# Performance work log

Measured on AMD Instinct MI355X. Metric: run time of the kernel, lower is better.

The kernel has to match this reference:

```python
import jax, jax.numpy as jnp
import numpy as np
import math

L_S = 64  # segment length (factor)


def setup_inputs() -> dict:
    key = jax.random.key(0)
    kq, kk, kv = jax.random.split(key, 3)
    B, L, H, D = 4, 8192, 16, 64
    return {
        "queries": jax.random.normal(kq, (B, L, H, D), dtype=jnp.float32),
        "keys": jax.random.normal(kk, (B, L, H, D), dtype=jnp.float32),
        "values": jax.random.normal(kv, (B, L, H, D), dtype=jnp.float32),
        "attn_mask": 0,
    }


def reference(queries, keys, values, attn_mask):
    B, L, H, D = queries.shape
    Ls = L_S
    M = L // Ls  # L % Ls == 0 by construction, so addition_Q path is a no-op
    scale = 1.0 / math.sqrt(Ls * D)

    # segment: [B, M, Ls, H, D]
    sq = queries.reshape(B, M, Ls, H, D)
    sk = keys.reshape(B, M, Ls, H, D)
    sv = values.reshape(B, M, Ls, H, D)

    # rfft over head dim D, ortho norm -> [B, M, Ls, H, D//2+1] complex
    qf = jnp.fft.rfft(sq, axis=-1, norm="ortho")
    kf = jnp.fft.rfft(sk, axis=-1, norm="ortho")
    vf = jnp.fft.rfft(sv, axis=-1, norm="ortho")

    # complex segment correlation: [B, H, M, M]
    scores = jnp.einsum("bmlhd,bnlhd->bhmn", qf, jnp.conj(kf)) / math.sqrt(D)
    A = jax.nn.softmax(scale * jnp.abs(scores), axis=-1)  # real
    Ac = A.astype(qf.dtype)  # complex with zero imaginary part

    # complex weighted sum of value spectra: [B, M, Ls, H, D//2+1]
    Vf = jnp.einsum("bhmn,bnlhd->bmlhd", Ac, vf)
    V = jnp.fft.irfft(Vf, n=D, axis=-1, norm="ortho")  # real [B, M, Ls, H, D]
    return V.reshape(B, L, H, D)
```

## Files before the change

kernel.cpp:

```cpp
#include <hip/hip_runtime.h>
#include <cstdint>
#include <cstddef>


typedef short bf16x8 __attribute__((ext_vector_type(8)));
typedef float f32x4 __attribute__((ext_vector_type(4)));

__device__ __forceinline__ ushort f2bf(float f) {
    union { float f; uint32_t u; } v; v.f = f;
    uint32_t r = (v.u + 0x7FFFu + ((v.u >> 16) & 1u)) >> 16;
    return (ushort)r;
}

__device__ __forceinline__ float bf2f(ushort h) {
    union { uint32_t u; float f; } v; v.u = ((uint32_t)h) << 16;
    return v.f;
}

__global__ void k_gmat(ushort* __restrict__ GreH, ushort* __restrict__ GreL,
                       ushort* __restrict__ GimH, ushort* __restrict__ GimL) {
    const float lam = 1.0f / 32768.0f;
    const float c = 3.14159265358979323846f / 32.0f;
    for (int e = threadIdx.x + blockIdx.x * blockDim.x; e < 4096; e += blockDim.x * gridDim.x) {
        int d = e >> 6, dp = e & 63;
        int delta = d - dp;
        float re = 0.f, im = 0.f;
        for (int k = 0; k <= 32; ++k) {
            int r = ((k * delta) % 64 + 64) % 64;
            float ang = c * (float)r;
            re += cosf(ang);
            im -= sinf(ang);
        }
        re *= lam; im *= lam;
        ushort rh = f2bf(re);
        GreH[e] = rh;
        GreL[e] = f2bf(re - bf2f(rh));
        ushort ih = f2bf(im);
        GimH[e] = ih;
        GimL[e] = f2bf(im - bf2f(ih));
    }
}

__global__ __launch_bounds__(256) void k_prep_q(const float* __restrict__ Q, ushort* __restrict__ Qf) {
    int blk = blockIdx.x;
    int bh = blk >> 7, m = blk & 127;
    int b = bh >> 4, h = bh & 15;
    const float* qbase = Q + ((size_t)(b * 8192 + m * 64)) * 1024 + h * 64;
    ushort* obase = Qf + ((size_t)bh * 128 + m) * 4096;
    for (int idx = threadIdx.x; idx < 1024; idx += 256) {
        int l = idx >> 4, d4 = (idx & 15) * 4;
        float4 v = *(const float4*)(qbase + (size_t)l * 1024 + d4);
        ushort4 o; o.x = f2bf(v.x); o.y = f2bf(v.y); o.z = f2bf(v.z); o.w = f2bf(v.w);
        *(ushort4*)(obase + idx * 4) = o;
    }
}

__global__ __launch_bounds__(256) void k_prep_k(const float* __restrict__ K,
                                                const ushort* __restrict__ GreH,
                                                const ushort* __restrict__ GreL,
                                                const ushort* __restrict__ GimH,
                                                const ushort* __restrict__ GimL,
                                                ushort* __restrict__ Kre, ushort* __restrict__ Kim) {
    __shared__ ushort kb[64 * 72];
    int blk = blockIdx.x;
    int bh = blk >> 7, n = blk & 127;
    int b = bh >> 4, h = bh & 15;
    int t = threadIdx.x;
    int lane = t & 63, wave = t >> 6;
    int wm = wave >> 1, wn = wave & 1;
    int row16 = lane & 15, quad = lane >> 4;

    bf16x8 grh[2][2], grl[2][2], gih[2][2], gil[2][2];
    #pragma unroll
    for (int nt = 0; nt < 2; ++nt)
        #pragma unroll
        for (int kk = 0; kk < 2; ++kk) {
            int off = (wn * 32 + nt * 16 + row16) * 64 + kk * 32 + quad * 8;
            grh[nt][kk] = *(const bf16x8*)(GreH + off);
            grl[nt][kk] = *(const bf16x8*)(GreL + off);
            gih[nt][kk] = *(const bf16x8*)(GimH + off);
            gil[nt][kk] = *(const bf16x8*)(GimL + off);
        }

    {
        int rrow = t >> 2, rcol = (t & 3) * 16;
        const float* kbase = K + ((size_t)(b * 8192 + n * 64 + rrow)) * 1024 + h * 64 + rcol;
        ushort* lbase = &kb[rrow * 72 + rcol];
        #pragma unroll
        for (int c = 0; c < 4; ++c) {
            float4 v = *(const float4*)(kbase + c * 4);
            ushort4 o; o.x = f2bf(v.x); o.y = f2bf(v.y); o.z = f2bf(v.z); o.w = f2bf(v.w);
            *(ushort4*)(lbase + c * 4) = o;
        }
    }
    __syncthreads();

    f32x4 accre[2][2] = {};
    f32x4 accim[2][2] = {};
    #pragma unroll
    for (int kk = 0; kk < 2; ++kk) {
        bf16x8 a[2];
        #pragma unroll
        for (int mt = 0; mt < 2; ++mt)
            a[mt] = *(const bf16x8*)&kb[(wm * 32 + mt * 16 + row16) * 72 + kk * 32 + quad * 8];
        #pragma unroll
        for (int mt = 0; mt < 2; ++mt)
            #pragma unroll
            for (int nt = 0; nt < 2; ++nt) {
                accre[mt][nt] = __builtin_amdgcn_mfma_f32_16x16x32_bf16(a[mt], grh[nt][kk], accre[mt][nt], 0, 0, 0);
                accre[mt][nt] = __builtin_amdgcn_mfma_f32_16x16x32_bf16(a[mt], grl[nt][kk], accre[mt][nt], 0, 0, 0);
                accim[mt][nt] = __builtin_amdgcn_mfma_f32_16x16x32_bf16(a[mt], gih[nt][kk], accim[mt][nt], 0, 0, 0);
                accim[mt][nt] = __builtin_amdgcn_mfma_f32_16x16x32_bf16(a[mt], gil[nt][kk], accim[mt][nt], 0, 0, 0);
            }
    }

    ushort* reb = Kre + ((size_t)bh * 128 + n) * 4096;
    ushort* imb = Kim + ((size_t)bh * 128 + n) * 4096;
    #pragma unroll
    for (int mt = 0; mt < 2; ++mt)
        #pragma unroll
        for (int nt = 0; nt < 2; ++nt)
            #pragma unroll
            for (int i = 0; i < 4; ++i) {
                int l = wm * 32 + mt * 16 + quad * 4 + i;
                int d = wn * 32 + nt * 16 + row16;
                reb[l * 64 + d] = f2bf(accre[mt][nt][i]);
                imb[l * 64 + d] = f2bf(accim[mt][nt][i]);
            }
}

__global__ __launch_bounds__(256) void k_scores(const ushort* __restrict__ Qf,
                                                const ushort* __restrict__ Kre,
                                                const ushort* __restrict__ Kim,
                                                float* __restrict__ Sre, float* __restrict__ Sim) {
    __shared__ ushort qt[64 * 72], ret[64 * 72], imt[64 * 72];
    int bh = blockIdx.y;
    int mh = blockIdx.x >> 1, nh = blockIdx.x & 1;
    int m0 = mh * 64, n0 = nh * 64;
    int t = threadIdx.x;
    int lane = t & 63, wave = t >> 6;
    int wm = wave >> 1, wn = wave & 1;
    int row16 = lane & 15, quad = lane >> 4;
    f32x4 accre[2][2] = {};
    f32x4 accim[2][2] = {};
    const ushort* qg = Qf + ((size_t)bh * 128 + m0) * 4096;
    const ushort* rg = Kre + ((size_t)bh * 128 + n0) * 4096;
    const ushort* ig = Kim + ((size_t)bh * 128 + n0) * 4096;
    for (int kt = 0; kt < 64; ++kt) {
        int j0 = kt * 64;
        #pragma unroll
        for (int p = 0; p < 2; ++p) {
            int idx = p * 256 + t;
            int row = idx >> 3, ch = idx & 7;
            size_t go = (size_t)row * 4096 + j0 + ch * 8;
            int lo = row * 72 + ch * 8;
            *(uint4*)&qt[lo]  = *(const uint4*)(qg + go);
            *(uint4*)&ret[lo] = *(const uint4*)(rg + go);
            *(uint4*)&imt[lo] = *(const uint4*)(ig + go);
        }
        __syncthreads();
        #pragma unroll
        for (int kk = 0; kk < 2; ++kk) {
            bf16x8 a[2], br[2], bi[2];
            #pragma unroll
            for (int mt = 0; mt < 2; ++mt)
                a[mt] = *(const bf16x8*)&qt[(wm * 32 + mt * 16 + row16) * 72 + kk * 32 + quad * 8];
            #pragma unroll
            for (int nt = 0; nt < 2; ++nt) {
                br[nt] = *(const bf16x8*)&ret[(wn * 32 + nt * 16 + row16) * 72 + kk * 32 + quad * 8];
                bi[nt] = *(const bf16x8*)&imt[(wn * 32 + nt * 16 + row16) * 72 + kk * 32 + quad * 8];
            }
            #pragma unroll
            for (int mt = 0; mt < 2; ++mt)
                #pragma unroll
                for (int nt = 0; nt < 2; ++nt) {
                    accre[mt][nt] = __builtin_amdgcn_mfma_f32_16x16x32_bf16(a[mt], br[nt], accre[mt][nt], 0, 0, 0);
                    accim[mt][nt] = __builtin_amdgcn_mfma_f32_16x16x32_bf16(a[mt], bi[nt], accim[mt][nt], 0, 0, 0);
                }
        }
        __syncthreads();
    }
    float* sre = Sre + (size_t)bh * 16384;
    float* sim = Sim + (size_t)bh * 16384;
    #pragma unroll
    for (int mt = 0; mt < 2; ++mt)
        #pragma unroll
        for (int nt = 0; nt < 2; ++nt)
            #pragma unroll
            for (int i = 0; i < 4; ++i) {
                int r = m0 + wm * 32 + mt * 16 + quad * 4 + i;
                int c = n0 + wn * 32 + nt * 16 + row16;
                sre[r * 128 + c] = accre[mt][nt][i];
                sim[r * 128 + c] = accim[mt][nt][i];
            }
}

__global__ __launch_bounds__(128) void k_softmax(const float* __restrict__ Sre,
                                                 const float* __restrict__ Sim,
                                                 ushort* __restrict__ A) {
    __shared__ float redmax[2], redsum[2];
    int row = blockIdx.x;
    int t = threadIdx.x;
    size_t off = (size_t)row * 128 + t;
    float re = Sre[off], im = Sim[off];
    float lg = sqrtf(re * re + im * im);
    float v = lg;
    for (int o = 32; o > 0; o >>= 1) v = fmaxf(v, __shfl_xor(v, o));
    if ((t & 63) == 0) redmax[t >> 6] = v;
    __syncthreads();
    float mx = fmaxf(redmax[0], redmax[1]);
    float e = expf(lg - mx);
    float s = e;
    for (int o = 32; o > 0; o >>= 1) s += __shfl_xor(s, o);
    if ((t & 63) == 0) redsum[t >> 6] = s;
    __syncthreads();
    float tot = redsum[0] + redsum[1];
    A[off] = f2bf(e / tot);
}

__global__ __launch_bounds__(256) void k_vt(const float* __restrict__ V, ushort* __restrict__ Vt) {
    __shared__ float tile[64 * 68];
    int l = blockIdx.x, nh = blockIdx.y, bh = blockIdx.z;
    int b = bh >> 4, h = bh & 15;
    int t = threadIdx.x;
    int n = t & 63, dq = t >> 6;
    const float* vbase = V + ((size_t)(b * 8192 + (nh * 64 + n) * 64 + l)) * 1024 + h * 64;
    #pragma unroll
    for (int r = 0; r < 4; ++r) {
        int d0 = r * 16 + dq * 4;
        float4 v = *(const float4*)(vbase + d0);
        tile[(d0 + 0) * 68 + n] = v.x; tile[(d0 + 1) * 68 + n] = v.y;
        tile[(d0 + 2) * 68 + n] = v.z; tile[(d0 + 3) * 68 + n] = v.w;
    }
    __syncthreads();
    int d = t >> 2, cq = t & 3;
    __align__(16) ushort u[16];
    #pragma unroll
    for (int i = 0; i < 16; ++i) u[i] = f2bf(tile[d * 68 + cq * 16 + i]);
    ushort* ob = Vt + ((size_t)bh * 4096 + l * 64 + d) * 128 + nh * 64 + cq * 16;
    *(uint4*)(ob) = *(uint4*)&u[0];
    *(uint4*)(ob + 8) = *(uint4*)&u[8];
}

__global__ __launch_bounds__(256) void k_mix(const ushort* __restrict__ A,
                                             const ushort* __restrict__ Vt,
                                             float* __restrict__ Out) {
    __shared__ ushort At[128 * 136], Vtl[64 * 136];
    int jt = blockIdx.x, bh = blockIdx.y;
    int b = bh >> 4, h = bh & 15;
    int j0 = jt * 64;
    int t = threadIdx.x;
    int lane = t & 63, wave = t >> 6;
    int row16 = lane & 15, quad = lane >> 4;
    const ushort* ag = A + (size_t)bh * 16384;
    const ushort* vg = Vt + ((size_t)bh * 4096 + j0) * 128;
    #pragma unroll
    for (int p = 0; p < 8; ++p) {
        int idx = p * 256 + t;
        int row = idx >> 4, ch = idx & 15;
        *(uint4*)&At[row * 136 + ch * 8] = *(const uint4*)(ag + row * 128 + ch * 8);
    }
    #pragma unroll
    for (int p = 0; p < 4; ++p) {
        int idx = p * 256 + t;
        int row = idx >> 4, ch = idx & 15;
        *(uint4*)&Vtl[row * 136 + ch * 8] = *(const uint4*)(vg + (size_t)row * 128 + ch * 8);
    }
    __syncthreads();
    f32x4 acc[2][4] = {};
    #pragma unroll
    for (int kk = 0; kk < 4; ++kk) {
        bf16x8 a[2], bv[4];
        #pragma unroll
        for (int mt = 0; mt < 2; ++mt)
            a[mt] = *(const bf16x8*)&At[(wave * 32 + mt * 16 + row16) * 136 + kk * 32 + quad * 8];
        #pragma unroll
        for (int j2 = 0; j2 < 4; ++j2)
            bv[j2] = *(const bf16x8*)&Vtl[(j2 * 16 + row16) * 136 + kk * 32 + quad * 8];
        #pragma unroll
        for (int mt = 0; mt < 2; ++mt)
            #pragma unroll
            for (int j2 = 0; j2 < 4; ++j2)
                acc[mt][j2] = __builtin_amdgcn_mfma_f32_16x16x32_bf16(a[mt], bv[j2], acc[mt][j2], 0, 0, 0);
    }
    #pragma unroll
    for (int mt = 0; mt < 2; ++mt)
        #pragma unroll
        for (int j2 = 0; j2 < 4; ++j2)
            #pragma unroll
            for (int i = 0; i < 4; ++i) {
                int m = wave * 32 + mt * 16 + quad * 4 + i;
                int j = j0 + j2 * 16 + row16;
                int ll = j >> 6, d = j & 63;
                Out[((size_t)(b * 8192 + m * 64 + ll)) * 1024 + h * 64 + d] = acc[mt][j2][i];
            }
}

extern "C" void kernel_launch(void* const* d_in, const int* in_sizes, int n_in,
                              void* d_out, int out_size, void* d_ws, size_t ws_size,
                              hipStream_t stream) {
    const float* Q = (const float*)d_in[0];
    const float* K = (const float*)d_in[1];
    const float* V = (const float*)d_in[2];
    float* Out = (float*)d_out;
    char* ws = (char*)d_ws;
    ushort* GreH = (ushort*)ws;
    ushort* GreL = GreH + 4096;
    ushort* GimH = GreL + 4096;
    ushort* GimL = GimH + 4096;
    float* Sre  = (float*)(ws + 32768);
    float* Sim  = (float*)(ws + 32768 + 4194304);
    ushort* A   = (ushort*)(ws + 32768 + 2 * 4194304);
    ushort* Qf  = (ushort*)(ws + 32768 + 2 * 4194304 + 2097152);
    ushort* Kre = Qf + 33554432;
    ushort* Kim = Kre + 33554432;
    ushort* Vt  = Qf;

    k_gmat<<<16, 256, 0, stream>>>(GreH, GreL, GimH, GimL);
    k_prep_q<<<8192, 256, 0, stream>>>(Q, Qf);
    k_prep_k<<<8192, 256, 0, stream>>>(K, GreH, GreL, GimH, GimL, Kre, Kim);
    k_scores<<<dim3(4, 64), 256, 0, stream>>>(Qf, Kre, Kim, Sre, Sim);
    k_softmax<<<8192, 128, 0, stream>>>(Sre, Sim, A);
    k_vt<<<dim3(64, 2, 64), 256, 0, stream>>>(V, Vt);
    k_mix<<<dim3(64, 64), 256, 0, stream>>>(A, Vt, Out);
}
```

Baseline: 619.4 us.

## Replace real-part DFT matmul with raw K plus DC/Nyquist correction terms

The real part of the frequency-domain score is now computed from raw bf16 K, with two extra appended columns per row (parity-split sums for the DC and Nyquist corrections) instead of a dense real DFT matmul. This removes the Kre matmul and its store. The change also adds register prefetching in k_scores, has each block process several tiles in prep, vt, softmax and mix, and rewrites softmax as one wave per row. The appended columns and rescaling change numerics slightly, and the larger per-block work lowers grid parallelism.

```diff
diff --git a/kernel.cpp b/kernel.cpp
--- a/kernel.cpp
+++ b/kernel.cpp
@@ -17,120 +17,131 @@
     return v.f;
 }
 
-__global__ void k_gmat(ushort* __restrict__ GreH, ushort* __restrict__ GreL,
-                       ushort* __restrict__ GimH, ushort* __restrict__ GimL) {
+__global__ void k_gmat(ushort* __restrict__ GimH, ushort* __restrict__ GimL) {
     const float lam = 1.0f / 32768.0f;
     const float c = 3.14159265358979323846f / 32.0f;
     for (int e = threadIdx.x + blockIdx.x * blockDim.x; e < 4096; e += blockDim.x * gridDim.x) {
         int d = e >> 6, dp = e & 63;
         int delta = d - dp;
-        float re = 0.f, im = 0.f;
+        float im = 0.f;
         for (int k = 0; k <= 32; ++k) {
             int r = ((k * delta) % 64 + 64) % 64;
-            float ang = c * (float)r;
-            re += cosf(ang);
-            im -= sinf(ang);
-        }
-        re *= lam; im *= lam;
-        ushort rh = f2bf(re);
-        GreH[e] = rh;
-        GreL[e] = f2bf(re - bf2f(rh));
+            im -= sinf(c * (float)r);
+        }
+        im *= lam;
         ushort ih = f2bf(im);
         GimH[e] = ih;
         GimL[e] = f2bf(im - bf2f(ih));
     }
 }
 
+#define PSCALE 0.17677669529663687f
+
 __global__ __launch_bounds__(256) void k_prep_q(const float* __restrict__ Q, ushort* __restrict__ Qf) {
-    int blk = blockIdx.x;
-    int bh = blk >> 7, m = blk & 127;
-    int b = bh >> 4, h = bh & 15;
-    const float* qbase = Q + ((size_t)(b * 8192 + m * 64)) * 1024 + h * 64;
-    ushort* obase = Qf + ((size_t)bh * 128 + m) * 4096;
-    for (int idx = threadIdx.x; idx < 1024; idx += 256) {
-        int l = idx >> 4, d4 = (idx & 15) * 4;
-        float4 v = *(const float4*)(qbase + (size_t)l * 1024 + d4);
-        ushort4 o; o.x = f2bf(v.x); o.y = f2bf(v.y); o.z = f2bf(v.z); o.w = f2bf(v.w);
-        *(ushort4*)(obase + idx * 4) = o;
+    int t = threadIdx.x;
+    for (int it = 0; it < 8; ++it) {
+        int g = blockIdx.x * 8 + it;
+        int bh = g >> 7, m = g & 127;
+        int b = bh >> 4, h = bh & 15;
+        const float* qbase = Q + ((size_t)(b * 8192 + m * 64)) * 1024 + h * 64;
+        ushort* obase = Qf + ((size_t)bh * 128 + m) * 4224;
+        #pragma unroll
+        for (int k = 0; k < 4; ++k) {
+            int idx = k * 256 + t;
+            int l = idx >> 4, d4 = (idx & 15) * 4;
+            float4 v = *(const float4*)(qbase + (size_t)l * 1024 + d4);
+            ushort4 o; o.x = f2bf(v.x); o.y = f2bf(v.y); o.z = f2bf(v.z); o.w = f2bf(v.w);
+            *(ushort4*)(obase + l * 64 + d4) = o;
+            float pe = v.x + v.z, po = v.y + v.w;
+            pe += __shfl_xor(pe, 1); po += __shfl_xor(po, 1);
+            pe += __shfl_xor(pe, 2); po += __shfl_xor(po, 2);
+            pe += __shfl_xor(pe, 4); po += __shfl_xor(po, 4);
+            pe += __shfl_xor(pe, 8); po += __shfl_xor(po, 8);
+            if ((t & 15) == 0) {
+                ushort2 pp; pp.x = f2bf(pe * PSCALE); pp.y = f2bf(po * PSCALE);
+                *(ushort2*)(obase + 4096 + 2 * l) = pp;
+            }
+        }
     }
 }
 
 __global__ __launch_bounds__(256) void k_prep_k(const float* __restrict__ K,
-                                                const ushort* __restrict__ GreH,
-                                                const ushort* __restrict__ GreL,
                                                 const ushort* __restrict__ GimH,
                                                 const ushort* __restrict__ GimL,
-                                                ushort* __restrict__ Kre, ushort* __restrict__ Kim) {
+                                                ushort* __restrict__ Kf, ushort* __restrict__ Kim) {
     __shared__ ushort kb[64 * 72];
-    int blk = blockIdx.x;
-    int bh = blk >> 7, n = blk & 127;
-    int b = bh >> 4, h = bh & 15;
     int t = threadIdx.x;
     int lane = t & 63, wave = t >> 6;
     int wm = wave >> 1, wn = wave & 1;
     int row16 = lane & 15, quad = lane >> 4;
-
-    bf16x8 grh[2][2], grl[2][2], gih[2][2], gil[2][2];
+    int rrow = t >> 2, rcol = (t & 3) * 16;
+
+    bf16x8 gih[2][2], gil[2][2];
     #pragma unroll
     for (int nt = 0; nt < 2; ++nt)
         #pragma unroll
         for (int kk = 0; kk < 2; ++kk) {
             int off = (wn * 32 + nt * 16 + row16) * 64 + kk * 32 + quad * 8;
-            grh[nt][kk] = *(const bf16x8*)(GreH + off);
-            grl[nt][kk] = *(const bf16x8*)(GreL + off);
             gih[nt][kk] = *(const bf16x8*)(GimH + off);
             gil[nt][kk] = *(const bf16x8*)(GimL + off);
         }
 
-    {
-        int rrow = t >> 2, rcol = (t & 3) * 16;
+    for (int it = 0; it < 8; ++it) {
+        int g = blockIdx.x * 8 + it;
+        int bh = g >> 7, n = g & 127;
+        int b = bh >> 4, h = bh & 15;
         const float* kbase = K + ((size_t)(b * 8192 + n * 64 + rrow)) * 1024 + h * 64 + rcol;
-        ushort* lbase = &kb[rrow * 72 + rcol];
+        ushort* kfrow = Kf + ((size_t)bh * 128 + n) * 4224;
+        float pe = 0.f, po = 0.f;
         #pragma unroll
         for (int c = 0; c < 4; ++c) {
             float4 v = *(const float4*)(kbase + c * 4);
             ushort4 o; o.x = f2bf(v.x); o.y = f2bf(v.y); o.z = f2bf(v.z); o.w = f2bf(v.w);
-            *(ushort4*)(lbase + c * 4) = o;
-        }
-    }
-    __syncthreads();
-
-    f32x4 accre[2][2] = {};
-    f32x4 accim[2][2] = {};
-    #pragma unroll
-    for (int kk = 0; kk < 2; ++kk) {
-        bf16x8 a[2];
+            *(ushort4*)&kb[rrow * 72 + rcol + c * 4] = o;
+            *(ushort4*)(kfrow + rrow * 64 + rcol + c * 4) = o;
+            pe += v.x + v.z; po += v.y + v.w;
+        }
+        pe += __shfl_xor(pe, 1); po += __shfl_xor(po, 1);
+        pe += __shfl_xor(pe, 2); po += __shfl_xor(po, 2);
+        if ((t & 3) == 0) {
+            ushort2 pp; pp.x = f2bf(pe * PSCALE); pp.y = f2bf(po * PSCALE);
+            *(ushort2*)(kfrow + 4096 + 2 * rrow) = pp;
+        }
+        __syncthreads();
+
+        f32x4 acc[2][2] = {};
+        #pragma unroll
+        for (int kk = 0; kk < 2; ++kk) {
+            bf16x8 a[2];
+            #pragma unroll
+            for (int mt = 0; mt < 2; ++mt)
+                a[mt] = *(const bf16x8*)&kb[(wm * 32 + mt * 16 + row16) * 72 + kk * 32 + quad * 8];
+            #pragma unroll
+            for (int mt = 0; mt < 2; ++mt)
+                #pragma unroll
+                for (int nt = 0; nt < 2; ++nt) {
+                    acc[mt][nt] = __builtin_amdgcn_mfma_f32_16x16x32_bf16(a[mt], gih[nt][kk], acc[mt][nt], 0, 0, 0);
+                    acc[mt][nt] = __builtin_amdgcn_mfma_f32_16x16x32_bf16(a[mt], gil[nt][kk], acc[mt][nt], 0, 0, 0);
+                }
+        }
+        __syncthreads();
         #pragma unroll
         for (int mt = 0; mt < 2; ++mt)
-            a[mt] = *(const bf16x8*)&kb[(wm * 32 + mt * 16 + row16) * 72 + kk * 32 + quad * 8];
-        #pragma unroll
-        for (int mt = 0; mt < 2; ++mt)
-            #pragma unroll
-            for (int nt = 0; nt < 2; ++nt) {
-                accre[mt][nt] = __builtin_amdgcn_mfma_f32_16x16x32_bf16(a[mt], grh[nt][kk], accre[mt][nt], 0, 0, 0);
-                accre[mt][nt] = __builtin_amdgcn_mfma_f32_16x16x32_bf16(a[mt], grl[nt][kk], accre[mt][nt], 0, 0, 0);
-                accim[mt][nt] = __builtin_amdgcn_mfma_f32_16x16x32_bf16(a[mt], gih[nt][kk], accim[mt][nt], 0, 0, 0);
-                accim[mt][nt] = __builtin_amdgcn_mfma_f32_16x16x32_bf16(a[mt], gil[nt][kk], accim[mt][nt], 0, 0, 0);
-            }
-    }
-
-    ushort* reb = Kre + ((size_t)bh * 128 + n) * 4096;
-    ushort* imb = Kim + ((size_t)bh * 128 + n) * 4096;
-    #pragma unroll
-    for (int mt = 0; mt < 2; ++mt)
-        #pragma unroll
-        for (int nt = 0; nt < 2; ++nt)
-            #pragma unroll
-            for (int i = 0; i < 4; ++i) {
-                int l = wm * 32 + mt * 16 + quad * 4 + i;
-                int d = wn * 32 + nt * 16 + row16;
-                reb[l * 64 + d] = f2bf(accre[mt][nt][i]);
-                imb[l * 64 + d] = f2bf(accim[mt][nt][i]);
-            }
+            #pragma unroll
+            for (int nt = 0; nt < 2; ++nt)
+                #pragma unroll
+                for (int i = 0; i < 4; ++i)
+                    kb[(wm * 32 + mt * 16 + quad * 4 + i) * 72 + wn * 32 + nt * 16 + row16] = f2bf(acc[mt][nt][i]);
+        __syncthreads();
+        ushort* kimrow = Kim + ((size_t)bh * 128 + n) * 4096;
+        *(uint4*)(kimrow + rrow * 64 + rcol)     = *(uint4*)&kb[rrow * 72 + rcol];
+        *(uint4*)(kimrow + rrow * 64 + rcol + 8) = *(uint4*)&kb[rrow * 72 + rcol + 8];
+        __syncthreads();
+    }
 }
 
 __global__ __launch_bounds__(256) void k_scores(const ushort* __restrict__ Qf,
-                                                const ushort* __restrict__ Kre,
+                                                const ushort* __restrict__ Kf,
                                                 const ushort* __restrict__ Kim,
                                                 float* __restrict__ Sre, float* __restrict__ Sim) {
     __shared__ ushort qt[64 * 72], ret[64 * 72], imt[64 * 72];
@@ -141,24 +152,43 @@
     int lane = t & 63, wave = t >> 6;
     int wm = wave >> 1, wn = wave & 1;
     int row16 = lane & 15, quad = lane >> 4;
+    const ushort* qg = Qf + ((size_t)bh * 128 + m0) * 4224;
+    const ushort* rg = Kf + ((size_t)bh * 128 + n0) * 4224;
+    const ushort* ig = Kim + ((size_t)bh * 128 + n0) * 4096;
+    uint4 rq[2], rk[2], ri[2];
+    #pragma unroll
+    for (int p = 0; p < 2; ++p) {
+        int idx = p * 256 + t;
+        int row = idx >> 3, ch = idx & 7;
+        rq[p] = *(const uint4*)(qg + (size_t)row * 4224 + ch * 8);
+        rk[p] = *(const uint4*)(rg + (size_t)row * 4224 + ch * 8);
+        ri[p] = *(const uint4*)(ig + (size_t)row * 4096 + ch * 8);
+    }
     f32x4 accre[2][2] = {};
     f32x4 accim[2][2] = {};
-    const ushort* qg = Qf + ((size_t)bh * 128 + m0) * 4096;
-    const ushort* rg = Kre + ((size_t)bh * 128 + n0) * 4096;
-    const ushort* ig = Kim + ((size_t)bh * 128 + n0) * 4096;
-    for (int kt = 0; kt < 64; ++kt) {
-        int j0 = kt * 64;
+    for (int kt = 0; kt < 66; ++kt) {
+        bool haveim = kt < 64;
         #pragma unroll
         for (int p = 0; p < 2; ++p) {
             int idx = p * 256 + t;
             int row = idx >> 3, ch = idx & 7;
-            size_t go = (size_t)row * 4096 + j0 + ch * 8;
             int lo = row * 72 + ch * 8;
-            *(uint4*)&qt[lo]  = *(const uint4*)(qg + go);
-            *(uint4*)&ret[lo] = *(const uint4*)(rg + go);
-            *(uint4*)&imt[lo] = *(const uint4*)(ig + go);
-        }
-        __syncthreads();
+            *(uint4*)&qt[lo] = rq[p];
+            *(uint4*)&ret[lo] = rk[p];
+            if (haveim) *(uint4*)&imt[lo] = ri[p];
+        }
+        __syncthreads();
+        if (kt + 1 < 66) {
+            int j0 = (kt + 1) * 64;
+            #pragma unroll
+            for (int p = 0; p < 2; ++p) {
+                int idx = p * 256 + t;
+                int row = idx >> 3, ch = idx & 7;
+                rq[p] = *(const uint4*)(qg + (size_t)row * 4224 + j0 + ch * 8);
+                rk[p] = *(const uint4*)(rg + (size_t)row * 4224 + j0 + ch * 8);
+                if (kt + 1 < 64) ri[p] = *(const uint4*)(ig + (size_t)row * 4096 + j0 + ch * 8);
+            }
+        }
         #pragma unroll
         for (int kk = 0; kk < 2; ++kk) {
             bf16x8 a[2], br[2], bi[2];
@@ -168,14 +198,15 @@
             #pragma unroll
             for (int nt = 0; nt < 2; ++nt) {
                 br[nt] = *(const bf16x8*)&ret[(wn * 32 + nt * 16 + row16) * 72 + kk * 32 + quad * 8];
-                bi[nt] = *(const bf16x8*)&imt[(wn * 32 + nt * 16 + row16) * 72 + kk * 32 + quad * 8];
+                if (haveim) bi[nt] = *(const bf16x8*)&imt[(wn * 32 + nt * 16 + row16) * 72 + kk * 32 + quad * 8];
             }
             #pragma unroll
             for (int mt = 0; mt < 2; ++mt)
                 #pragma unroll
                 for (int nt = 0; nt < 2; ++nt) {
                     accre[mt][nt] = __builtin_amdgcn_mfma_f32_16x16x32_bf16(a[mt], br[nt], accre[mt][nt], 0, 0, 0);
-                    accim[mt][nt] = __builtin_amdgcn_mfma_f32_16x16x32_bf16(a[mt], bi[nt], accim[mt][nt], 0, 0, 0);
+                    if (haveim)
+                        accim[mt][nt] = __builtin_amdgcn_mfma_f32_16x16x32_bf16(a[mt], bi[nt], accim[mt][nt], 0, 0, 0);
                 }
         }
         __syncthreads();
@@ -190,110 +221,117 @@
             for (int i = 0; i < 4; ++i) {
                 int r = m0 + wm * 32 + mt * 16 + quad * 4 + i;
                 int c = n0 + wn * 32 + nt * 16 + row16;
-                sre[r * 128 + c] = accre[mt][nt][i];
+                sre[r * 128 + c] = accre[mt][nt][i] * 0.0009765625f;
                 sim[r * 128 + c] = accim[mt][nt][i];
             }
 }
 
-__global__ __launch_bounds__(128) void k_softmax(const float* __restrict__ Sre,
+__global__ __launch_bounds__(256) void k_softmax(const float* __restrict__ Sre,
                                                  const float* __restrict__ Sim,
                                                  ushort* __restrict__ A) {
-    __shared__ float redmax[2], redsum[2];
-    int row = blockIdx.x;
-    int t = threadIdx.x;
-    size_t off = (size_t)row * 128 + t;
-    float re = Sre[off], im = Sim[off];
-    float lg = sqrtf(re * re + im * im);
-    float v = lg;
-    for (int o = 32; o > 0; o >>= 1) v = fmaxf(v, __shfl_xor(v, o));
-    if ((t & 63) == 0) redmax[t >> 6] = v;
-    __syncthreads();
-    float mx = fmaxf(redmax[0], redmax[1]);
-    float e = expf(lg - mx);
-    float s = e;
-    for (int o = 32; o > 0; o >>= 1) s += __shfl_xor(s, o);
-    if ((t & 63) == 0) redsum[t >> 6] = s;
-    __syncthreads();
-    float tot = redsum[0] + redsum[1];
-    A[off] = f2bf(e / tot);
+    int t = threadIdx.x;
+    int lane = t & 63, wave = t >> 6;
+    for (int it = 0; it < 4; ++it) {
+        int row = blockIdx.x * 16 + it * 4 + wave;
+        size_t off = (size_t)row * 128 + lane * 2;
+        float2 re = *(const float2*)(Sre + off);
+        float2 im = *(const float2*)(Sim + off);
+        float lg0 = sqrtf(re.x * re.x + im.x * im.x);
+        float lg1 = sqrtf(re.y * re.y + im.y * im.y);
+        float mx = fmaxf(lg0, lg1);
+        for (int o = 32; o > 0; o >>= 1) mx = fmaxf(mx, __shfl_xor(mx, o));
+        float e0 = expf(lg0 - mx), e1 = expf(lg1 - mx);
+        float s = e0 + e1;
+        for (int o = 32; o > 0; o >>= 1) s += __shfl_xor(s, o);
+        float inv = 1.0f / s;
+        ushort2 o2; o2.x = f2bf(e0 * inv); o2.y = f2bf(e1 * inv);
+        *(ushort2*)(A + off) = o2;
+    }
 }
 
 __global__ __launch_bounds__(256) void k_vt(const float* __restrict__ V, ushort* __restrict__ Vt) {
     __shared__ float tile[64 * 68];
-    int l = blockIdx.x, nh = blockIdx.y, bh = blockIdx.z;
+    int lg = blockIdx.x, nh = blockIdx.y, bh = blockIdx.z;
     int b = bh >> 4, h = bh & 15;
     int t = threadIdx.x;
     int n = t & 63, dq = t >> 6;
-    const float* vbase = V + ((size_t)(b * 8192 + (nh * 64 + n) * 64 + l)) * 1024 + h * 64;
-    #pragma unroll
-    for (int r = 0; r < 4; ++r) {
-        int d0 = r * 16 + dq * 4;
-        float4 v = *(const float4*)(vbase + d0);
-        tile[(d0 + 0) * 68 + n] = v.x; tile[(d0 + 1) * 68 + n] = v.y;
-        tile[(d0 + 2) * 68 + n] = v.z; tile[(d0 + 3) * 68 + n] = v.w;
-    }
-    __syncthreads();
     int d = t >> 2, cq = t & 3;
-    __align__(16) ushort u[16];
-    #pragma unroll
-    for (int i = 0; i < 16; ++i) u[i] = f2bf(tile[d * 68 + cq * 16 + i]);
-    ushort* ob = Vt + ((size_t)bh * 4096 + l * 64 + d) * 128 + nh * 64 + cq * 16;
-    *(uint4*)(ob) = *(uint4*)&u[0];
-    *(uint4*)(ob + 8) = *(uint4*)&u[8];
+    for (int it = 0; it < 4; ++it) {
+        int l = lg * 4 + it;
+        const float* vbase = V + ((size_t)(b * 8192 + (nh * 64 + n) * 64 + l)) * 1024 + h * 64;
+        #pragma unroll
+        for (int r = 0; r < 4; ++r) {
+            int d0 = r * 16 + dq * 4;
+            float4 v = *(const float4*)(vbase + d0);
+            tile[(d0 + 0) * 68 + n] = v.x; tile[(d0 + 1) * 68 + n] = v.y;
+            tile[(d0 + 2) * 68 + n] = v.z; tile[(d0 + 3) * 68 + n] = v.w;
+        }
+        __syncthreads();
+        __align__(16) ushort u[16];
+        #pragma unroll
+        for (int i = 0; i < 16; ++i) u[i] = f2bf(tile[d * 68 + cq * 16 + i]);
+        ushort* ob = Vt + ((size_t)bh * 4096 + l * 64 + d) * 128 + nh * 64 + cq * 16;
+        *(uint4*)(ob) = *(uint4*)&u[0];
+        *(uint4*)(ob + 8) = *(uint4*)&u[8];
+        __syncthreads();
+    }
 }
 
 __global__ __launch_bounds__(256) void k_mix(const ushort* __restrict__ A,
                                              const ushort* __restrict__ Vt,
                                              float* __restrict__ Out) {
     __shared__ ushort At[128 * 136], Vtl[64 * 136];
-    int jt = blockIdx.x, bh = blockIdx.y;
+    int grp = blockIdx.x, bh = blockIdx.y;
     int b = bh >> 4, h = bh & 15;
-    int j0 = jt * 64;
     int t = threadIdx.x;
     int lane = t & 63, wave = t >> 6;
     int row16 = lane & 15, quad = lane >> 4;
     const ushort* ag = A + (size_t)bh * 16384;
-    const ushort* vg = Vt + ((size_t)bh * 4096 + j0) * 128;
     #pragma unroll
     for (int p = 0; p < 8; ++p) {
         int idx = p * 256 + t;
         int row = idx >> 4, ch = idx & 15;
         *(uint4*)&At[row * 136 + ch * 8] = *(const uint4*)(ag + row * 128 + ch * 8);
     }
-    #pragma unroll
-    for (int p = 0; p < 4; ++p) {
-        int idx = p * 256 + t;
-        int row = idx >> 4, ch = idx & 15;
-        *(uint4*)&Vtl[row * 136 + ch * 8] = *(const uint4*)(vg + (size_t)row * 128 + ch * 8);
-    }
-    __syncthreads();
-    f32x4 acc[2][4] = {};
-    #pragma unroll
-    for (int kk = 0; kk < 4; ++kk) {
-        bf16x8 a[2], bv[4];
+    for (int jt8 = 0; jt8 < 8; ++jt8) {
+        int jt = grp * 8 + jt8;
+        int j0 = jt * 64;
+        const ushort* vg = Vt + ((size_t)bh * 4096 + j0) * 128;
+        __syncthreads();
+        #pragma unroll
+        for (int p = 0; p < 4; ++p) {
+            int idx = p * 256 + t;
+            int row = idx >> 4, ch = idx & 15;
+            *(uint4*)&Vtl[row * 136 + ch * 8] = *(const uint4*)(vg + (size_t)row * 128 + ch * 8);
+        }
+        __syncthreads();
+        f32x4 acc[2][4] = {};
+        #pragma unroll
+        for (int kk = 0; kk < 4; ++kk) {
+            bf16x8 a[2], bv[4];
+            #pragma unroll
+            for (int mt = 0; mt < 2; ++mt)
+                a[mt] = *(const bf16x8*)&At[(wave * 32 + mt * 16 + row16) * 136 + kk * 32 + quad * 8];
+            #pragma unroll
+            for (int j2 = 0; j2 < 4; ++j2)
+                bv[j2] = *(const bf16x8*)&Vtl[(j2 * 16 + row16) * 136 + kk * 32 + quad * 8];
+            #pragma unroll
+            for (int mt = 0; mt < 2; ++mt)
+                #pragma unroll
+                for (int j2 = 0; j2 < 4; ++j2)
+                    acc[mt][j2] = __builtin_amdgcn_mfma_f32_16x16x32_bf16(a[mt], bv[j2], acc[mt][j2], 0, 0, 0);
+        }
         #pragma unroll
         for (int mt = 0; mt < 2; ++mt)
-            a[mt] = *(const bf16x8*)&At[(wave * 32 + mt * 16 + row16) * 136 + kk * 32 + quad * 8];
-        #pragma unroll
-        for (int j2 = 0; j2 < 4; ++j2)
-            bv[j2] = *(const bf16x8*)&Vtl[(j2 * 16 + row16) * 136 + kk * 32 + quad * 8];
-        #pragma unroll
-        for (int mt = 0; mt < 2; ++mt)
             #pragma unroll
             for (int j2 = 0; j2 < 4; ++j2)
-                acc[mt][j2] = __builtin_amdgcn_mfma_f32_16x16x32_bf16(a[mt], bv[j2], acc[mt][j2], 0, 0, 0);
-    }
-    #pragma unroll
-    for (int mt = 0; mt < 2; ++mt)
-        #pragma unroll
-        for (int j2 = 0; j2 < 4; ++j2)
-            #pragma unroll
-            for (int i = 0; i < 4; ++i) {
-                int m = wave * 32 + mt * 16 + quad * 4 + i;
-                int j = j0 + j2 * 16 + row16;
-                int ll = j >> 6, d = j & 63;
-                Out[((size_t)(b * 8192 + m * 64 + ll)) * 1024 + h * 64 + d] = acc[mt][j2][i];
-            }
+                #pragma unroll
+                for (int i = 0; i < 4; ++i) {
+                    int m = wave * 32 + mt * 16 + quad * 4 + i;
+                    int dd = j2 * 16 + row16;
+                    Out[((size_t)(b * 8192 + m * 64 + jt)) * 1024 + h * 64 + dd] = acc[mt][j2][i];
+                }
+    }
 }
 
 extern "C" void kernel_launch(void* const* d_in, const int* in_sizes, int n_in,
@@ -304,23 +342,21 @@
     const float* V = (const float*)d_in[2];
     float* Out = (float*)d_out;
     char* ws = (char*)d_ws;
-    ushort* GreH = (ushort*)ws;
-    ushort* GreL = GreH + 4096;
-    ushort* GimH = GreL + 4096;
+    ushort* GimH = (ushort*)ws;
     ushort* GimL = GimH + 4096;
     float* Sre  = (float*)(ws + 32768);
     float* Sim  = (float*)(ws + 32768 + 4194304);
     ushort* A   = (ushort*)(ws + 32768 + 2 * 4194304);
     ushort* Qf  = (ushort*)(ws + 32768 + 2 * 4194304 + 2097152);
-    ushort* Kre = Qf + 33554432;
-    ushort* Kim = Kre + 33554432;
+    ushort* Kf  = Qf + (size_t)64 * 128 * 4224;
+    ushort* Kim = Kf + (size_t)64 * 128 * 4224;
     ushort* Vt  = Qf;
 
-    k_gmat<<<16, 256, 0, stream>>>(GreH, GreL, GimH, GimL);
-    k_prep_q<<<8192, 256, 0, stream>>>(Q, Qf);
-    k_prep_k<<<8192, 256, 0, stream>>>(K, GreH, GreL, GimH, GimL, Kre, Kim);
-    k_scores<<<dim3(4, 64), 256, 0, stream>>>(Qf, Kre, Kim, Sre, Sim);
-    k_softmax<<<8192, 128, 0, stream>>>(Sre, Sim, A);
-    k_vt<<<dim3(64, 2, 64), 256, 0, stream>>>(V, Vt);
-    k_mix<<<dim3(64, 64), 256, 0, stream>>>(A, Vt, Out);
-}
+    k_gmat<<<16, 256, 0, stream>>>(GimH, GimL);
+    k_prep_q<<<1024, 256, 0, stream>>>(Q, Qf);
+    k_prep_k<<<1024, 256, 0, stream>>>(K, GimH, GimL, Kf, Kim);
+    k_scores<<<dim3(4, 64), 256, 0, stream>>>(Qf, Kf, Kim, Sre, Sim);
+    k_softmax<<<512, 256, 0, stream>>>(Sre, Sim, A);
+    k_vt<<<dim3(16, 2, 64), 256, 0, stream>>>(V, Vt);
+    k_mix<<<dim3(8, 64), 256, 0, stream>>>(A, Vt, Out);
+}
```

Measured after the change: 645.3 us. 1.04x slower.
